# Optimization experiments

Hardware: AMD Instinct MI355X
Metric: run time of the kernel (lower is better)

## Reference

```python
import jax, jax.numpy as jnp
import numpy as np

NUM_CLASSES = 81
THRESHOLD = 0.5
NEGPOS_RATIO = 3
VARIANCE = (0.1, 0.2)


def point_form(p):
    # center-size -> corner form
    return jnp.concatenate([p[:, :2] - p[:, 2:] / 2, p[:, :2] + p[:, 2:] / 2], axis=1)


def jaccard(box_a, box_b):
    # box_a: [O,4] corners, box_b: [P,4] corners -> IoU [O,P]
    lt = jnp.maximum(box_a[:, None, :2], box_b[None, :, :2])
    rb = jnp.minimum(box_a[:, None, 2:], box_b[None, :, 2:])
    wh = jnp.clip(rb - lt, 0.0)
    inter = wh[..., 0] * wh[..., 1]
    area_a = ((box_a[:, 2] - box_a[:, 0]) * (box_a[:, 3] - box_a[:, 1]))[:, None]
    area_b = ((box_b[:, 2] - box_b[:, 0]) * (box_b[:, 3] - box_b[:, 1]))[None, :]
    return inter / (area_a + area_b - inter)


def encode(matched, priors, variances):
    # matched: [P,4] corner GT, priors: [P,4] center-size
    g_cxcy = (matched[:, :2] + matched[:, 2:]) / 2 - priors[:, :2]
    g_cxcy = g_cxcy / (variances[0] * priors[:, 2:])
    g_wh = (matched[:, 2:] - matched[:, :2]) / priors[:, 2:]
    g_wh = jnp.log(g_wh) / variances[1]
    return jnp.concatenate([g_cxcy, g_wh], axis=1)


def match_one(truths, labels, priors):
    overlaps = jaccard(truths, point_form(priors))   # [O,P]
    best_prior_idx = jnp.argmax(overlaps, axis=1)     # [O] best prior per truth
    best_truth_overlap = jnp.max(overlaps, axis=0)    # [P]
    best_truth_idx = jnp.argmax(overlaps, axis=0)     # [P] best truth per prior
    # force each truth's best prior to match that truth
    best_truth_overlap = best_truth_overlap.at[best_prior_idx].set(2.0)
    best_truth_idx = best_truth_idx.at[best_prior_idx].set(jnp.arange(truths.shape[0]))
    matched = truths[best_truth_idx]                  # [P,4]
    conf = labels[best_truth_idx].astype(jnp.int32) + 1
    conf = jnp.where(best_truth_overlap < THRESHOLD, 0, conf)
    loc = encode(matched, priors, VARIANCE)
    return loc, conf


def _loss(loc_data, conf_data, targets, priors):
    B, P, C = conf_data.shape
    loc_t, conf_t = jax.vmap(lambda t: match_one(t[:, :4], t[:, 4], priors))(targets)
    pos = conf_t > 0                                  # [B,P]
    # smooth-L1 (beta=1) over positive priors, sum reduction
    d = loc_data - loc_t
    sl1 = jnp.where(jnp.abs(d) < 1.0, 0.5 * d * d, jnp.abs(d) - 0.5)
    loss_l = jnp.sum(jnp.where(pos[..., None], sl1, 0.0))
    # per-prior CE used both for mining ranking and the final conf loss
    ce = jax.nn.logsumexp(conf_data, axis=-1) - jnp.take_along_axis(
        conf_data, conf_t[..., None], axis=-1)[..., 0]   # [B,P]
    # hard negative mining: zero positives, double argsort for rank
    loss_c_rank = jnp.where(pos, 0.0, ce)
    loss_idx = jnp.argsort(-loss_c_rank, axis=1)
    idx_rank = jnp.argsort(loss_idx, axis=1)
    num_pos = jnp.sum(pos, axis=1, keepdims=True)     # [B,1]
    num_neg = jnp.minimum(NEGPOS_RATIO * num_pos, P - 1)
    neg = idx_rank < num_neg
    sel = pos | neg
    loss_c = jnp.sum(jnp.where(sel, ce, 0.0))
    N = jnp.sum(num_pos).astype(loc_data.dtype)
    return loss_l / N, loss_c / N


def setup_inputs():
    key = jax.random.key(0)
    kl, kc, kb1, kb2, kll, kp1, kp2 = jax.random.split(key, 7)
    B, P, O, C = 64, 8732, 50, NUM_CLASSES
    loc_data = jax.random.normal(kl, (B, P, 4), jnp.float32)
    conf_data = jax.random.normal(kc, (B, P, C), jnp.float32)
    # valid GT boxes in corner form inside [0,1]
    cxcy = jax.random.uniform(kb1, (B, O, 2), minval=0.2, maxval=0.8)
    wh = jax.random.uniform(kb2, (B, O, 2), minval=0.05, maxval=0.3)
    boxes = jnp.concatenate([cxcy - wh / 2, cxcy + wh / 2], axis=-1)
    labels = jax.random.randint(kll, (B, O), 0, C - 1).astype(jnp.float32)
    targets = jnp.concatenate([boxes, labels[..., None]], axis=-1)  # [B,O,5]
    # priors in center-size form
    pcxcy = jax.random.uniform(kp1, (P, 2), minval=0.05, maxval=0.95)
    pwh = jax.random.uniform(kp2, (P, 2), minval=0.05, maxval=0.5)
    priors = jnp.concatenate([pcxcy, pwh], axis=-1)
    return {"loc_data": loc_data, "conf_data": conf_data, "targets": targets, "priors": priors}


def reference(loc_data, conf_data, targets, priors):
    return _loss(loc_data, conf_data, targets, priors)
```

## Files before the change

### kernel.cpp

```cpp
#include <hip/hip_runtime.h>
#include <float.h>

#pragma clang fp contract(off)

typedef unsigned long long ull;
typedef unsigned int u32;

#define THRESH 0.5f
#define PPT 4
#define SEL_T 512
#define ENC_SEG 1024
#define LSE_ROWS 128


__device__ __forceinline__ float sl1(float d) {
    float a = fabsf(d);
    return (a < 1.f) ? 0.5f * d * d : a - 0.5f;
}

__device__ __forceinline__ void gload16(const void* g, void* l) {
    __builtin_amdgcn_global_load_lds(
        (const __attribute__((address_space(1))) void*)g,
        (__attribute__((address_space(3))) void*)l, 16, 0, 0);
}
__device__ __forceinline__ void gload4(const void* g, void* l) {
    __builtin_amdgcn_global_load_lds(
        (const __attribute__((address_space(1))) void*)g,
        (__attribute__((address_space(3))) void*)l, 4, 0, 0);
}

__global__ __launch_bounds__(256) void k_prep(
        const float* __restrict__ targets, const float* __restrict__ priors,
        const float* __restrict__ conf,
        float* __restrict__ bto, int* __restrict__ bti, ull* __restrict__ tbest,
        float* __restrict__ lse,
        u32* __restrict__ zws, int nz,
        int P, int O, int S, int SB, int SPEC, int G, int npairs, long long BP) {
    __shared__ __align__(16) float smem[LSE_ROWS * 81];
    const int bid = blockIdx.x;
    if (bid == 0)
        for (int i = threadIdx.x; i < nz; i += 256) zws[i] = 0;

    long long t0 = (long long)bid * SPEC;
    int k0 = (int)(t0 / G);
    bool is_spec = (int)((t0 + SPEC) / G) > k0;

    if (!is_spec) {
        const int lb = bid - k0;
        const long long r0 = (long long)lb * LSE_ROWS;
        const int w = threadIdx.x >> 6;
        const int lane = threadIdx.x & 63;
        const char* gbase = (const char*)(conf + r0 * 81);

        if (r0 + LSE_ROWS <= BP) {
            for (int i = w * 10; i < w * 10 + 10; i++)
                gload16(gbase + (size_t)i * 1024 + lane * 16, (char*)smem + i * 1024);
            if (w == 0) {
                gload4(gbase + 40960 + lane * 4, (char*)smem + 40960);
                gload4(gbase + 41216 + lane * 4, (char*)smem + 41216);
            }
            asm volatile("s_waitcnt vmcnt(0)" ::: "memory");
        } else {
            int nfl = (int)(BP - r0) * 81;
            const float* src = (const float*)gbase;
            for (int i = threadIdx.x; i < nfl; i += 256) smem[i] = src[i];
        }
        __syncthreads();

        const int row = threadIdx.x >> 1;
        const int half = threadIdx.x & 1;
        if (r0 + row < BP) {
            const float* rp = smem + row * 81;
            const int c0 = half * 41;
            const int cn = half ? 40 : 41;
            float sum = 0.f;
            for (int j = 0; j < cn; j++) sum += __expf(rp[c0 + j]);
            sum += __shfl_xor(sum, 1);
            if (half == 0) lse[r0 + row] = __logf(sum);
        }
        return;
    }

    const int sidx = k0;
    if (sidx < SB) {
        float4* tbox = (float4*)smem;
        float*  tarea = smem + 512;
        const int b = sidx / S, seg = sidx % S;
        const float* trow = targets + (size_t)b * O * 5;
        for (int o = threadIdx.x; o < O; o += 256) {
            float x1 = trow[o * 5 + 0], y1 = trow[o * 5 + 1];
            float x2 = trow[o * 5 + 2], y2 = trow[o * 5 + 3];
            tbox[o] = make_float4(x1, y1, x2, y2);
            tarea[o] = (x2 - x1) * (y2 - y1);
        }
        __syncthreads();
        const int p0 = seg * (256 * PPT);
        float px1[PPT], py1[PPT], px2[PPT], py2[PPT], pa[PPT];
        float bestv[PPT]; int besto[PPT]; int pidx[PPT];
#pragma unroll
        for (int j = 0; j < PPT; j++) {
            int p = p0 + (int)threadIdx.x + j * 256;
            pidx[j] = p; bestv[j] = -1.f; besto[j] = 0;
            if (p < P) {
                float4 pr = ((const float4*)priors)[p];
                px1[j] = pr.x - pr.z / 2.f;
                py1[j] = pr.y - pr.w / 2.f;
                px2[j] = pr.x + pr.z / 2.f;
                py2[j] = pr.y + pr.w / 2.f;
                pa[j] = (px2[j] - px1[j]) * (py2[j] - py1[j]);
            } else {
                px1[j] = 2.f; py1[j] = 2.f; px2[j] = 2.f; py2[j] = 2.f; pa[j] = 1.f;
            }
        }
        for (int o = 0; o < O; o++) {
            float4 t = tbox[o];
            float ta = tarea[o];
#pragma unroll
            for (int j = 0; j < PPT; j++) {
                float lx = fmaxf(t.x, px1[j]), ly = fmaxf(t.y, py1[j]);
                float rx = fminf(t.z, px2[j]), ry = fminf(t.w, py2[j]);
                float wx = fmaxf(rx - lx, 0.f), wy = fmaxf(ry - ly, 0.f);
                float inter = wx * wy;
                float iou = 0.f;
                if (inter > 0.f) iou = inter / (ta + pa[j] - inter);
                if (iou > bestv[j]) { bestv[j] = iou; besto[j] = o; }
            }
        }
#pragma unroll
        for (int j = 0; j < PPT; j++) {
            if (pidx[j] < P) {
                bto[(size_t)b * P + pidx[j]] = bestv[j];
                bti[(size_t)b * P + pidx[j]] = besto[j];
            }
        }
    } else {
        int g = (sidx - SB) * 4 + ((int)threadIdx.x >> 6);
        int lane = threadIdx.x & 63;
        if (g >= npairs) return;
        int OP = (O + 1) >> 1;
        int b = g / OP;
        int o0 = (g % OP) * 2;
        const float* trow = targets + ((size_t)b * O + o0) * 5;
        float ax1 = trow[0], ay1 = trow[1], ax2 = trow[2], ay2 = trow[3];
        float ta0 = (ax2 - ax1) * (ay2 - ay1);
        bool has1 = (o0 + 1) < O;
        float cx1 = 0, cy1 = 0, cx2 = 0, cy2 = 0, ta1 = 1.f;
        if (has1) {
            cx1 = trow[5]; cy1 = trow[6]; cx2 = trow[7]; cy2 = trow[8];
            ta1 = (cx2 - cx1) * (cy2 - cy1);
        }
        ull k0v = 0, k1v = 0;
        for (int p = lane; p < P; p += 64) {
            float4 pr = ((const float4*)priors)[p];
            float bx1 = pr.x - pr.z / 2.f;
            float by1 = pr.y - pr.w / 2.f;
            float bx2 = pr.x + pr.z / 2.f;
            float by2 = pr.y + pr.w / 2.f;
            float pa = (bx2 - bx1) * (by2 - by1);
            u32 np = ~(u32)p;
            {
                float lx = fmaxf(ax1, bx1), ly = fmaxf(ay1, by1);
                float rx = fminf(ax2, bx2), ry = fminf(ay2, by2);
                float wx = fmaxf(rx - lx, 0.f), wy = fmaxf(ry - ly, 0.f);
                float inter = wx * wy;
                float iou = 0.f;
                if (inter > 0.f) iou = inter / (ta0 + pa - inter);
                ull key = ((ull)__float_as_uint(iou) << 32) | np;
                if (key > k0v) k0v = key;
            }
            if (has1) {
                float lx = fmaxf(cx1, bx1), ly = fmaxf(cy1, by1);
                float rx = fminf(cx2, bx2), ry = fminf(cy2, by2);
                float wx = fmaxf(rx - lx, 0.f), wy = fmaxf(ry - ly, 0.f);
                float inter = wx * wy;
                float iou = 0.f;
                if (inter > 0.f) iou = inter / (ta1 + pa - inter);
                ull key = ((ull)__float_as_uint(iou) << 32) | np;
                if (key > k1v) k1v = key;
            }
        }
        for (int off = 32; off; off >>= 1) {
            ull a = __shfl_xor(k0v, off); if (a > k0v) k0v = a;
            ull d = __shfl_xor(k1v, off); if (d > k1v) k1v = d;
        }
        if (lane == 0) {
            tbest[(size_t)b * O + o0] = k0v;
            if (has1) tbest[(size_t)b * O + o0 + 1] = k1v;
        }
    }
}

__global__ __launch_bounds__(256) void k_encode_ce(
        const float* __restrict__ targets, const float* __restrict__ priors,
        const float* __restrict__ loc_data, const float* __restrict__ conf,
        const ull* __restrict__ tbest, const float* __restrict__ lse,
        float* __restrict__ F,
        int* __restrict__ conf_t,
        int* __restrict__ num_pos, float* __restrict__ loss_l,
        int P, int O) {
    const int b = blockIdx.y, seg = blockIdx.x;
    __shared__ float tr[64 * 5];
    __shared__ int ov[ENC_SEG];
    __shared__ float redf[4]; __shared__ int redi[4];
    const int p0 = seg * ENC_SEG;
    const int p1 = min(p0 + ENC_SEG, P);
    const int nprior = p1 - p0;
    const float* trow = targets + (size_t)b * O * 5;
    for (int i = threadIdx.x; i < O * 5; i += 256) tr[i] = trow[i];
    for (int i = threadIdx.x; i < nprior; i += 256) ov[i] = -1;
    __syncthreads();
    if ((int)threadIdx.x < O) {
        ull tb = tbest[(size_t)b * O + threadIdx.x];
        u32 p = ~(u32)(tb & 0xFFFFFFFFULL);
        if (p >= (u32)P) p = 0;
        if ((int)p >= p0 && (int)p < p1) atomicMax(&ov[p - p0], (int)threadIdx.x);
    }
    __syncthreads();
    float ll = 0.f; int cnt = 0;
    for (int p = p0 + (int)threadIdx.x; p < p1; p += 256) {
        size_t idx = (size_t)b * P + p;
        int o = conf_t[idx];
        int ovv = ov[p - p0];
        bool forced = ovv >= 0;
        if (forced) o = ovv;
        float ovl = F[idx];
        int cv = (!forced && ovl < THRESH) ? 0 : ((int)tr[o * 5 + 4] + 1);
        conf_t[idx] = cv;
        if (cv > 0) {
            cnt++;
            float4 pr = ((const float4*)priors)[p];
            float mx1 = tr[o * 5], my1 = tr[o * 5 + 1];
            float mx2 = tr[o * 5 + 2], my2 = tr[o * 5 + 3];
            float gx = ((mx1 + mx2) / 2.f - pr.x) / (0.1f * pr.z);
            float gy = ((my1 + my2) / 2.f - pr.y) / (0.1f * pr.w);
            float gw = logf((mx2 - mx1) / pr.z) / 0.2f;
            float gh = logf((my2 - my1) / pr.w) / 0.2f;
            float4 ld = ((const float4*)loc_data)[idx];
            ll += sl1(ld.x - gx) + sl1(ld.y - gy) + sl1(ld.z - gw) + sl1(ld.w - gh);
        }
        float tv = conf[idx * 81 + cv];
        F[idx] = lse[idx] - tv;
    }
    for (int off = 32; off; off >>= 1) {
        ll += __shfl_down(ll, off);
        cnt += __shfl_down(cnt, off);
    }
    int w = threadIdx.x >> 6;
    if ((threadIdx.x & 63) == 0) { redf[w] = ll; redi[w] = cnt; }
    __syncthreads();
    if (threadIdx.x == 0) {
        float l = 0; int c = 0;
        for (int i = 0; i < 4; i++) { l += redf[i]; c += redi[i]; }
        if (c) atomicAdd(&num_pos[b], c);
        atomicAdd(&loss_l[b], l);
    }
}

__global__ __launch_bounds__(SEL_T) void k_select(
        const float* __restrict__ ce, const int* __restrict__ conf_t,
        const int* __restrict__ num_pos, const float* __restrict__ loss_l,
        float* __restrict__ acc, u32* __restrict__ ticket,
        float* __restrict__ out, int P, int B) {
    extern __shared__ u32 sk[];
    __shared__ u32 whist[SEL_T / 64][16];
    __shared__ u32 hist[16];
    __shared__ float redf[SEL_T / 64]; __shared__ u32 redu[SEL_T / 64];
    __shared__ u32 sh_pval; __shared__ int sh_rem;
    const int b = blockIdx.x;
    const size_t base = (size_t)b * P;
    const int lane = threadIdx.x & 63;
    const int w = threadIdx.x >> 6;
    const int NW = SEL_T / 64;

    float ps = 0.f;
    for (int p = threadIdx.x; p < P; p += SEL_T) {
        int c = conf_t[base + p];
        float v = ce[base + p];
        u32 key;
        if (c > 0) { ps += v; key = 0u; }
        else key = __float_as_uint(fmaxf(v, 0.f));
        sk[p] = key;
    }
    for (int off = 32; off; off >>= 1) ps += __shfl_down(ps, off);
    if (lane == 0) redf[w] = ps;
    __syncthreads();
    float pos_sum = 0.f;
    if (threadIdx.x == 0) {
        for (int i = 0; i < NW; i++) pos_sum += redf[i];
    }

    const int np = num_pos[b];
    const int k = min(3 * np, P - 1);
    u32 pval = 0, pmask = 0; int rem = k;
    if (k > 0) {
        for (int shift = 28; shift >= 0; shift -= 4) {
            __syncthreads();
            ull a0 = 0, a1 = 0;
            for (int p = threadIdx.x; p < P; p += SEL_T) {
                u32 key = sk[p];
                if ((key & pmask) == pval) {
                    u32 dig = (key >> shift) & 15u;
                    ull inc = 1ull << ((dig & 7u) * 8u);
                    if (dig < 8u) a0 += inc; else a1 += inc;
                }
            }
            const ull M = 0x00FF00FF00FF00FFull;
            ull e0 = a0 & M, e1 = (a0 >> 8) & M, e2 = a1 & M, e3 = (a1 >> 8) & M;
            for (int off = 32; off; off >>= 1) {
                e0 += __shfl_xor(e0, off);
                e1 += __shfl_xor(e1, off);
                e2 += __shfl_xor(e2, off);
                e3 += __shfl_xor(e3, off);
            }
            if (lane == 0) {
#pragma unroll
                for (int j = 0; j < 4; j++) {
                    whist[w][2 * j]     = (u32)((e0 >> (16 * j)) & 0xFFFF);
                    whist[w][2 * j + 1] = (u32)((e1 >> (16 * j)) & 0xFFFF);
                    whist[w][8 + 2 * j]     = (u32)((e2 >> (16 * j)) & 0xFFFF);
                    whist[w][8 + 2 * j + 1] = (u32)((e3 >> (16 * j)) & 0xFFFF);
                }
            }
            __syncthreads();
            if (threadIdx.x < 16) {
                u32 h = 0;
                for (int i = 0; i < NW; i++) h += whist[i][threadIdx.x];
                hist[threadIdx.x] = h;
            }
            __syncthreads();
            if (threadIdx.x == 0) {
                u32 accu = 0; int d = 15;
                for (; d > 0; d--) {
                    u32 h = hist[d];
                    if (accu + h >= (u32)rem) break;
                    accu += h;
                }
                sh_pval = pval | ((u32)d << shift);
                sh_rem = rem - (int)accu;
            }
            __syncthreads();
            pval = sh_pval; rem = sh_rem; pmask |= (0xFu << shift);
        }
    }

    float sgt = 0.f; u32 cgt = 0;
    if (k > 0) {
        for (int p = threadIdx.x; p < P; p += SEL_T) {
            u32 key = sk[p];
            if (key > pval) { sgt += __uint_as_float(key); cgt++; }
        }
    }
    for (int off = 32; off; off >>= 1) {
        sgt += __shfl_down(sgt, off);
        cgt += __shfl_down(cgt, off);
    }
    __syncthreads();
    if (lane == 0) { redf[w] = sgt; redu[w] = cgt; }
    __syncthreads();
    if (threadIdx.x == 0) {
        float s = 0.f; u32 c = 0;
        for (int i = 0; i < NW; i++) { s += redf[i]; c += redu[i]; }
        float t = __uint_as_float(pval);
        float lc_b = pos_sum + ((k > 0) ? (s + (float)(k - (int)c) * t) : 0.f);
        atomicAdd(&acc[0], (float)np);
        atomicAdd(&acc[1], loss_l[b]);
        atomicAdd(&acc[2], lc_b);
        __threadfence();
        u32 tk = atomicAdd(ticket, 1u);
        if (tk == (u32)(B - 1)) {
            float n  = atomicAdd(&acc[0], 0.f);
            float ll = atomicAdd(&acc[1], 0.f);
            float lc = atomicAdd(&acc[2], 0.f);
            out[0] = ll / n;
            out[1] = lc / n;
        }
    }
}


extern "C" void kernel_launch(void* const* d_in, const int* in_sizes, int n_in,
                              void* d_out, int out_size, void* d_ws, size_t ws_size,
                              hipStream_t stream) {
    const float* loc     = (const float*)d_in[0];
    const float* conf    = (const float*)d_in[1];
    const float* targets = (const float*)d_in[2];
    const float* priors  = (const float*)d_in[3];

    const int P = in_sizes[3] / 4;
    const int B = in_sizes[0] / (P * 4);
    const int O = in_sizes[2] / (B * 5);
    const long long BP = (long long)B * P;

    char* ws = (char*)d_ws;
    size_t off = 0;
    int*   num_pos = (int*)(ws + off);   off += (size_t)B * sizeof(int);
    float* loss_l  = (float*)(ws + off); off += (size_t)B * sizeof(float);
    float* acc     = (float*)(ws + off); off += 4 * sizeof(float);
    u32*   ticket  = (u32*)(ws + off);   off += sizeof(u32);
    const int zwords = (int)(off >> 2);
    off = (off + 7) & ~(size_t)7;
    ull*   tbest   = (ull*)(ws + off);   off += (size_t)B * O * sizeof(ull);
    float* F       = (float*)(ws + off); off += (size_t)BP * sizeof(float);
    int*   I       = (int*)(ws + off);   off += (size_t)BP * sizeof(int);
    float* L       = (float*)(ws + off); off += (size_t)BP * sizeof(float);

    const int SEG = 256 * PPT;
    const int S = (P + SEG - 1) / SEG;
    const int SB = S * B;
    const int npairs = B * ((O + 1) / 2);
    const int TB = (npairs + 3) / 4;
    const int CB = (int)((BP + LSE_ROWS - 1) / LSE_ROWS);
    const int SPEC = SB + TB;
    const int G = CB + SPEC;
    k_prep<<<G, 256, 0, stream>>>(targets, priors, conf, F, I, tbest, L,
                                  (u32*)ws, zwords, P, O, S, SB, SPEC, G, npairs, BP);

    const int S2 = (P + ENC_SEG - 1) / ENC_SEG;
    k_encode_ce<<<dim3(S2, B), 256, 0, stream>>>(targets, priors, loc, conf, tbest, L,
                                                 F, I, num_pos, loss_l, P, O);

    k_select<<<B, SEL_T, (size_t)P * sizeof(u32), stream>>>(F, I, num_pos, loss_l,
                                                            acc, ticket, (float*)d_out, P, B);
}
```

Before: 359.7 us.

## Make LSE blocks persistent with double-buffered async LDS tile loads

The log-sum-exp stage of k_prep now uses a fixed set of 512 persistent 128-thread blocks. Each block loops over 64-row tiles of conf and double-buffers them in LDS through async global-to-LDS loads, with partial vmcnt waits so the next tile loads while the current one is reduced. The old interleaved mapping of special blocks (matching and best-prior work) among LSE blocks is replaced by placing them after the LSE blocks, with block size halved and priors per thread doubled. The intent is to hide memory latency on the bandwidth-heavy conf read. The cost is fewer resident blocks and correctness that depends on the hand-tuned vmcnt counts.

```diff
diff --git a/kernel.cpp b/kernel.cpp
--- a/kernel.cpp
+++ b/kernel.cpp
@@ -7,10 +7,12 @@
 typedef unsigned int u32;
 
 #define THRESH 0.5f
-#define PPT 4
 #define SEL_T 512
 #define ENC_SEG 1024
-#define LSE_ROWS 128
+#define TILE_ROWS 64
+#define TILE_B 20736
+#define NLSE 512
+#define PPT2 8
 
 
 __device__ __forceinline__ float sl1(float d) {
@@ -29,77 +31,88 @@
         (__attribute__((address_space(3))) void*)l, 4, 0, 0);
 }
 
-__global__ __launch_bounds__(256) void k_prep(
+__global__ __launch_bounds__(128) void k_prep(
         const float* __restrict__ targets, const float* __restrict__ priors,
         const float* __restrict__ conf,
         float* __restrict__ bto, int* __restrict__ bti, ull* __restrict__ tbest,
         float* __restrict__ lse,
         u32* __restrict__ zws, int nz,
-        int P, int O, int S, int SB, int SPEC, int G, int npairs, long long BP) {
-    __shared__ __align__(16) float smem[LSE_ROWS * 81];
+        int P, int O, int S, int SB, int npairs, int ntiles, long long BP) {
+    __shared__ __align__(16) float smem[2 * TILE_ROWS * 81];
     const int bid = blockIdx.x;
-    if (bid == 0)
-        for (int i = threadIdx.x; i < nz; i += 256) zws[i] = 0;
-
-    long long t0 = (long long)bid * SPEC;
-    int k0 = (int)(t0 / G);
-    bool is_spec = (int)((t0 + SPEC) / G) > k0;
-
-    if (!is_spec) {
-        const int lb = bid - k0;
-        const long long r0 = (long long)lb * LSE_ROWS;
-        const int w = threadIdx.x >> 6;
-        const int lane = threadIdx.x & 63;
-        const char* gbase = (const char*)(conf + r0 * 81);
-
-        if (r0 + LSE_ROWS <= BP) {
-            for (int i = w * 10; i < w * 10 + 10; i++)
-                gload16(gbase + (size_t)i * 1024 + lane * 16, (char*)smem + i * 1024);
-            if (w == 0) {
-                gload4(gbase + 40960 + lane * 4, (char*)smem + 40960);
-                gload4(gbase + 41216 + lane * 4, (char*)smem + 41216);
-            }
-            asm volatile("s_waitcnt vmcnt(0)" ::: "memory");
-        } else {
-            int nfl = (int)(BP - r0) * 81;
-            const float* src = (const float*)gbase;
-            for (int i = threadIdx.x; i < nfl; i += 256) smem[i] = src[i];
-        }
-        __syncthreads();
-
-        const int row = threadIdx.x >> 1;
-        const int half = threadIdx.x & 1;
-        if (r0 + row < BP) {
-            const float* rp = smem + row * 81;
-            const int c0 = half * 41;
-            const int cn = half ? 40 : 41;
-            float sum = 0.f;
-            for (int j = 0; j < cn; j++) sum += __expf(rp[c0 + j]);
-            sum += __shfl_xor(sum, 1);
-            if (half == 0) lse[r0 + row] = __logf(sum);
-        }
+    const int tid = threadIdx.x;
+    const int w = tid >> 6;
+    const int lane = tid & 63;
+
+    if (bid < NLSE) {
+        if (bid == 0)
+            for (int i = tid; i < nz; i += 128) zws[i] = 0;
+
+        const int nt = (ntiles - bid + NLSE - 1) / NLSE;
+        if (nt <= 0) return;
+
+        #define STAGE(T, BI) do {                                            \
+            const char* g_ = (const char*)conf + (size_t)(T) * TILE_B;       \
+            char* l_ = (char*)smem + (BI) * TILE_B;                          \
+            _Pragma("unroll")                                                \
+            for (int c_ = 0; c_ < 10; c_++) {                                \
+                int i_ = w * 10 + c_;                                        \
+                gload16(g_ + (size_t)i_ * 1024 + lane * 16, l_ + i_ * 1024); \
+            }                                                                \
+            if (w == 0) gload4(g_ + 20480 + lane * 4, l_ + 20480);           \
+        } while (0)
+
+        STAGE(bid, 0);
+        if (nt > 1) STAGE(bid + NLSE, 1);
+
+        const int row = tid >> 1;
+        const int half = tid & 1;
+        const int c0 = half * 41;
+        const int cn = half ? 40 : 41;
+
+        for (int i = 0; i < nt; i++) {
+            const int t = bid + i * NLSE;
+            if (i >= nt - 2) {
+                asm volatile("s_waitcnt vmcnt(0)" ::: "memory");
+            } else {
+                asm volatile("s_waitcnt vmcnt(10)" ::: "memory");
+            }
+            __builtin_amdgcn_s_barrier();
+
+            const float* rp = smem + (i & 1) * (TILE_ROWS * 81) + row * 81;
+            long long r = (long long)t * TILE_ROWS + row;
+            if (r < BP) {
+                float sum = 0.f;
+                for (int j = 0; j < cn; j++) sum += __expf(rp[c0 + j]);
+                sum += __shfl_xor(sum, 1);
+                if (half == 0) lse[r] = __logf(sum);
+            }
+            __builtin_amdgcn_s_barrier();
+            if (i + 2 < nt) STAGE(bid + (i + 2) * NLSE, (i & 1));
+        }
+        #undef STAGE
         return;
     }
 
-    const int sidx = k0;
+    const int sidx = bid - NLSE;
     if (sidx < SB) {
         float4* tbox = (float4*)smem;
         float*  tarea = smem + 512;
         const int b = sidx / S, seg = sidx % S;
         const float* trow = targets + (size_t)b * O * 5;
-        for (int o = threadIdx.x; o < O; o += 256) {
+        for (int o = tid; o < O; o += 128) {
             float x1 = trow[o * 5 + 0], y1 = trow[o * 5 + 1];
             float x2 = trow[o * 5 + 2], y2 = trow[o * 5 + 3];
             tbox[o] = make_float4(x1, y1, x2, y2);
             tarea[o] = (x2 - x1) * (y2 - y1);
         }
         __syncthreads();
-        const int p0 = seg * (256 * PPT);
-        float px1[PPT], py1[PPT], px2[PPT], py2[PPT], pa[PPT];
-        float bestv[PPT]; int besto[PPT]; int pidx[PPT];
+        const int p0 = seg * (128 * PPT2);
+        float px1[PPT2], py1[PPT2], px2[PPT2], py2[PPT2], pa[PPT2];
+        float bestv[PPT2]; int besto[PPT2]; int pidx[PPT2];
 #pragma unroll
-        for (int j = 0; j < PPT; j++) {
-            int p = p0 + (int)threadIdx.x + j * 256;
+        for (int j = 0; j < PPT2; j++) {
+            int p = p0 + tid + j * 128;
             pidx[j] = p; bestv[j] = -1.f; besto[j] = 0;
             if (p < P) {
                 float4 pr = ((const float4*)priors)[p];
@@ -116,7 +129,7 @@
             float4 t = tbox[o];
             float ta = tarea[o];
 #pragma unroll
-            for (int j = 0; j < PPT; j++) {
+            for (int j = 0; j < PPT2; j++) {
                 float lx = fmaxf(t.x, px1[j]), ly = fmaxf(t.y, py1[j]);
                 float rx = fminf(t.z, px2[j]), ry = fminf(t.w, py2[j]);
                 float wx = fmaxf(rx - lx, 0.f), wy = fmaxf(ry - ly, 0.f);
@@ -127,15 +140,14 @@
             }
         }
 #pragma unroll
-        for (int j = 0; j < PPT; j++) {
+        for (int j = 0; j < PPT2; j++) {
             if (pidx[j] < P) {
                 bto[(size_t)b * P + pidx[j]] = bestv[j];
                 bti[(size_t)b * P + pidx[j]] = besto[j];
             }
         }
     } else {
-        int g = (sidx - SB) * 4 + ((int)threadIdx.x >> 6);
-        int lane = threadIdx.x & 63;
+        int g = (sidx - SB) * 2 + w;
         if (g >= npairs) return;
         int OP = (O + 1) >> 1;
         int b = g / OP;
@@ -404,16 +416,15 @@
     int*   I       = (int*)(ws + off);   off += (size_t)BP * sizeof(int);
     float* L       = (float*)(ws + off); off += (size_t)BP * sizeof(float);
 
-    const int SEG = 256 * PPT;
+    const int ntiles = (int)((BP + TILE_ROWS - 1) / TILE_ROWS);
+    const int SEG = 128 * PPT2;
     const int S = (P + SEG - 1) / SEG;
     const int SB = S * B;
     const int npairs = B * ((O + 1) / 2);
-    const int TB = (npairs + 3) / 4;
-    const int CB = (int)((BP + LSE_ROWS - 1) / LSE_ROWS);
-    const int SPEC = SB + TB;
-    const int G = CB + SPEC;
-    k_prep<<<G, 256, 0, stream>>>(targets, priors, conf, F, I, tbest, L,
-                                  (u32*)ws, zwords, P, O, S, SB, SPEC, G, npairs, BP);
+    const int TB = (npairs + 1) / 2;
+    const int G = NLSE + SB + TB;
+    k_prep<<<G, 128, 0, stream>>>(targets, priors, conf, F, I, tbest, L,
+                                  (u32*)ws, zwords, P, O, S, SB, npairs, ntiles, BP);
 
     const int S2 = (P + ENC_SEG - 1) / ENC_SEG;
     k_encode_ce<<<dim3(S2, B), 256, 0, stream>>>(targets, priors, loc, conf, tbest, L,
```

Result: slower. 389.4 us (+8.3%).
